# Kernel optimization log

Hardware: AMD Instinct MI355X
Metric: run time of the kernel (lower is better)

Reference implementation:

```python
import jax, jax.numpy as jnp
import numpy as np

HEAD_COUNT = 16
EMBED_DIM = 2048
B, S = 2, 2048


def setup_inputs() -> dict:
    key = jax.random.key(0)
    k1, k2, k3, k4, k5 = jax.random.split(key, 5)
    keys = jax.random.normal(k1, (B, S, EMBED_DIM), dtype=jnp.float32)
    values = jax.random.normal(k2, (B, S, EMBED_DIM), dtype=jnp.float32)
    queries = jax.random.normal(k3, (B, S, EMBED_DIM), dtype=jnp.float32)
    # padding-style mask; guarantee at least one valid key per batch row
    attention_mask = jax.random.randint(k4, (B, S), 0, 2).astype(bool)
    attention_mask = attention_mask.at[:, 0].set(True)
    w_out = jax.random.normal(k5, (EMBED_DIM, EMBED_DIM), dtype=jnp.float32) * (EMBED_DIM ** -0.5)
    return {"keys": keys, "values": values, "queries": queries,
            "attention_mask": attention_mask, "w_out": w_out}


def reference(keys, values, queries, attention_mask, w_out):
    b, s, e = queries.shape
    h = HEAD_COUNT
    c = e // h  # head dim
    k = keys.reshape(b, s, h, c)
    v = values.reshape(b, s, h, c)
    q = queries.reshape(b, s, h, c) * (c ** -0.5)
    # [B,H,Q,K] scores + additive padding bias on key axis
    scores = jnp.einsum('bqhc,bkhc->bhqk', q, k)
    bias = jnp.where(attention_mask, 0.0, -jnp.inf)[:, None, None, :]
    weights = jax.nn.softmax(scores + bias, axis=-1)
    out = jnp.einsum('bhqk,bkhc->bqhc', weights, v).reshape(b, s, e)
    # nn.Linear(bias=False): y = x @ W^T
    return out @ w_out.T
```

## Files before the change

kernel.cpp:

```cpp
#include <hip/hip_runtime.h>
#include <hip/hip_bf16.h>
#include <math.h>

#define B_ 2
#define S_ 2048
#define E_ 2048
#define H_ 16
#define C_ 128

typedef __attribute__((ext_vector_type(8))) short s8v;
typedef __attribute__((ext_vector_type(4))) float f32x4;
typedef __attribute__((ext_vector_type(2))) unsigned u32x2;
typedef __attribute__((ext_vector_type(4))) unsigned u32x4;

#define MFMA16(a, b, c) __builtin_amdgcn_mfma_f32_16x16x32_bf16((a), (b), (c), 0, 0, 0)

__device__ __forceinline__ unsigned fbits(float f) {
    union { float f; unsigned u; } v{f};
    return v.u;
}
__device__ __forceinline__ short f2bfh(float f) {
    return (short)((fbits(f) + 0x8000u) >> 16);
}
__device__ __forceinline__ unsigned bfpack(float lo, float hi) {
    return __builtin_amdgcn_perm(fbits(hi) + 0x8000u, fbits(lo) + 0x8000u, 0x07060302u);
}

__device__ __forceinline__ float fexp2(float x) {
    float r;
    asm("v_exp_f32 %0, %1" : "=v"(r) : "v"(x));
    return r;
}
__device__ __forceinline__ float frcp(float x) {
    float r;
    asm("v_rcp_f32 %0, %1" : "=v"(r) : "v"(x));
    return r;
}

__device__ __forceinline__ void glds16(const void* g, void* l) {
    __builtin_amdgcn_global_load_lds(
        (const __attribute__((address_space(1))) void*)g,
        (__attribute__((address_space(3))) void*)l, 16, 0, 0);
}

template <bool DOK>
__global__ __launch_bounds__(256) void prep_kv(
    const float* __restrict__ K, const float* __restrict__ V,
    short* __restrict__ Kb, short* __restrict__ Vt)
{
    __shared__ __align__(16) short vt[C_][66];
    const int t  = threadIdx.x;
    const int s0 = blockIdx.x * 64;
    const int bh = blockIdx.y;
    const int b = bh >> 4, h = bh & 15;

    if (DOK) {
#pragma unroll
        for (int i = 0; i < 8; ++i) {
            int idx = t + i * 256;
            int s = idx >> 5, c4 = idx & 31;
            float4 v = *(const float4*)(K + ((size_t)(b * S_ + s0 + s)) * E_ + h * C_ + c4 * 4);
            u32x2 o = {bfpack(v.x, v.y), bfpack(v.z, v.w)};
            *(u32x2*)(Kb + ((size_t)(bh * S_ + s0 + s)) * C_ + c4 * 4) = o;
        }
    }
#pragma unroll
    for (int i = 0; i < 8; ++i) {
        int idx = t + i * 256;
        int r = idx >> 5, c4 = idx & 31;
        float4 v = *(const float4*)(V + ((size_t)(b * S_ + s0 + r)) * E_ + h * C_ + c4 * 4);
        vt[c4 * 4 + 0][r] = f2bfh(v.x);
        vt[c4 * 4 + 1][r] = f2bfh(v.y);
        vt[c4 * 4 + 2][r] = f2bfh(v.z);
        vt[c4 * 4 + 3][r] = f2bfh(v.w);
    }
    __syncthreads();
#pragma unroll
    for (int i = 0; i < 4; ++i) {
        int idx = t + i * 256;
        int c = idx >> 3, sc = idx & 7;
        *(s8v*)(Vt + ((size_t)(bh * C_ + c)) * S_ + s0 + sc * 8) = *(const s8v*)&vt[c][sc * 8];
    }
}

__global__ __launch_bounds__(256) void convw_kernel(
    const float* __restrict__ W, short* __restrict__ Wb)
{
    size_t i = ((size_t)blockIdx.x * 256 + threadIdx.x) * 8;
    float4 a = *(const float4*)(W + i);
    float4 b = *(const float4*)(W + i + 4);
    u32x4 o = {bfpack(a.x, a.y), bfpack(a.z, a.w), bfpack(b.x, b.y), bfpack(b.z, b.w)};
    *(u32x4*)(Wb + i) = o;
}

constexpr int QT = 256;
constexpr int KT = 64;
constexpr float M0 = 16.0f;

template <bool KBF16>
__global__ __launch_bounds__(512, 2) void attn_mfma(
    const short* __restrict__ Kb, const float* __restrict__ Kf,
    const float* __restrict__ Qp, const short* __restrict__ Vt,
    const int* __restrict__ maskp, short* __restrict__ Op)
{
    __shared__ __align__(16) short ks[2][KT * 128];
    __shared__ __align__(16) short vs[2][C_ * 64];
    __shared__ __align__(16) short ps[8][16][72];

    const int t = threadIdx.x;
    const int w = t >> 6, lane = t & 63;
    const int c15 = lane & 15, quad = lane >> 4;
    const int q0 = blockIdx.x * QT;
    const int h = blockIdx.y, b = blockIdx.z;
    const int bh = b * H_ + h;

    const float qscale = 0.12751744458187936f;
    s8v qf[2][4];
#pragma unroll
    for (int mi = 0; mi < 2; ++mi) {
        const float* qrow = Qp + ((size_t)(b * S_ + q0 + w * 32 + mi * 16 + c15)) * E_ + h * C_;
#pragma unroll
        for (int kk = 0; kk < 4; ++kk) {
            const float* p = qrow + kk * 32 + quad * 8;
            float4 x0 = *(const float4*)p;
            float4 x1 = *(const float4*)(p + 4);
            u32x4 pk = {bfpack(x0.x * qscale, x0.y * qscale),
                        bfpack(x0.z * qscale, x0.w * qscale),
                        bfpack(x1.x * qscale, x1.y * qscale),
                        bfpack(x1.z * qscale, x1.w * qscale)};
            qf[mi][kk] = *(s8v*)&pk;
        }
    }

    s8v ones;
#pragma unroll
    for (int j = 0; j < 8; ++j) ones[j] = (short)0x3F80;

    f32x4 O[2][8], Ol[2];
#pragma unroll
    for (int mi = 0; mi < 2; ++mi) {
        Ol[mi] = (f32x4){0.f, 0.f, 0.f, 0.f};
#pragma unroll
        for (int ct = 0; ct < 8; ++ct) O[mi][ct] = (f32x4){0.f, 0.f, 0.f, 0.f};
    }

    const short* Kbh = Kb + (size_t)(bh * S_) * C_;
    const float* Kfh = Kf + (size_t)(b * S_) * E_ + h * C_;
    const short* Vbh = Vt + (size_t)(bh * C_) * S_;
    const int*   mptr = maskp + b * S_ + 4 * c15;

    int kgp[4], vgp[2];
#pragma unroll
    for (int kk = 0; kk < 4; ++kk) kgp[kk] = ((4 * kk + quad) ^ c15) * 8;
#pragma unroll
    for (int ks2 = 0; ks2 < 2; ++ks2) vgp[ks2] = ((4 * ks2 + quad) ^ (c15 & 7)) * 8;

    auto stage = [&](short* ksb, short* vsb, int k0) {
        const int r4 = lane >> 4, gp = lane & 15;
#pragma unroll
        for (int i = 0; i < 2; ++i) {
            int row = w * 8 + i * 4 + r4;
            int g = gp ^ ((row >> 2) & 15);
            glds16(Kbh + (size_t)(k0 + row) * C_ + g * 8, ksb + (w * 8 + i * 4) * 128);
        }
        const int cr = lane >> 3, gp7 = lane & 7;
#pragma unroll
        for (int i = 0; i < 2; ++i) {
            int c = w * 16 + i * 8 + cr;
            int g = gp7 ^ (c & 7);
            glds16(Vbh + (size_t)c * S_ + k0 + g * 8, vsb + (w * 16 + i * 8) * 64);
        }
    };

    auto compute = [&](const short* ksc, const short* vsc, int4 mv) {
        float bva[4] = {mv.x ? -M0 : -1e30f, mv.y ? -M0 : -1e30f,
                        mv.z ? -M0 : -1e30f, mv.w ? -M0 : -1e30f};
        f32x4 Sf[2][4];
        __builtin_amdgcn_s_setprio(1);
#pragma unroll
        for (int nt = 0; nt < 4; ++nt) {
            f32x4 s0 = (f32x4){bva[nt], bva[nt], bva[nt], bva[nt]};
            f32x4 s1 = s0;
            const short* krow = ksc + (4 * c15 + nt) * 128;
#pragma unroll
            for (int kk = 0; kk < 4; ++kk) {
                s8v bf = *(const s8v*)(krow + kgp[kk]);
                s0 = MFMA16(qf[0][kk], bf, s0);
                s1 = MFMA16(qf[1][kk], bf, s1);
            }
            Sf[0][nt] = s0; Sf[1][nt] = s1;
        }
        __builtin_amdgcn_s_setprio(0);

        s8v af[2][2];
#pragma unroll
        for (int mi = 0; mi < 2; ++mi) {
#pragma unroll
            for (int r = 0; r < 4; ++r) {
                float p0 = fexp2(Sf[mi][0][r]);
                float p1 = fexp2(Sf[mi][1][r]);
                float p2 = fexp2(Sf[mi][2][r]);
                float p3 = fexp2(Sf[mi][3][r]);
                u32x2 d = {bfpack(p0, p1), bfpack(p2, p3)};
                *(u32x2*)&ps[w][quad * 4 + r][4 * c15] = d;
            }
#pragma unroll
            for (int ks2 = 0; ks2 < 2; ++ks2)
                af[mi][ks2] = *(const s8v*)&ps[w][c15][ks2 * 32 + quad * 8];
        }

        __builtin_amdgcn_s_setprio(1);
#pragma unroll
        for (int ct = 0; ct < 8; ++ct) {
            const short* vrow = vsc + (ct * 16 + c15) * 64;
#pragma unroll
            for (int ks2 = 0; ks2 < 2; ++ks2) {
                s8v bf = *(const s8v*)(vrow + vgp[ks2]);
                O[0][ct] = MFMA16(af[0][ks2], bf, O[0][ct]);
                O[1][ct] = MFMA16(af[1][ks2], bf, O[1][ct]);
            }
        }
#pragma unroll
        for (int mi = 0; mi < 2; ++mi) {
            Ol[mi] = MFMA16(af[mi][0], ones, Ol[mi]);
            Ol[mi] = MFMA16(af[mi][1], ones, Ol[mi]);
        }
        __builtin_amdgcn_s_setprio(0);
    };

    if (KBF16) {
        stage(&ks[0][0], &vs[0][0], 0);
        int4 mcur = *(const int4*)mptr;
        __syncthreads();
#pragma unroll 1
        for (int k0 = 0; k0 < S_; k0 += 2 * KT) {
            stage(&ks[1][0], &vs[1][0], k0 + KT);
            int4 m1 = *(const int4*)(mptr + k0 + KT);
            compute(&ks[0][0], &vs[0][0], mcur);
            __syncthreads();

            int4 m2 = m1;
            if (k0 + 2 * KT < S_) {
                stage(&ks[0][0], &vs[0][0], k0 + 2 * KT);
                m2 = *(const int4*)(mptr + k0 + 2 * KT);
            }
            compute(&ks[1][0], &vs[1][0], m1);
            mcur = m2;
            __syncthreads();
        }
    } else {
#pragma unroll 1
        for (int k0 = 0; k0 < S_; k0 += KT) {
#pragma unroll
            for (int i = 0; i < 4; ++i) {
                int idx = t + i * 512;
                int r = idx >> 5, c4 = idx & 31;
                float4 kv = *(const float4*)(Kfh + (size_t)(k0 + r) * E_ + c4 * 4);
                u32x2 sv = {bfpack(kv.x, kv.y), bfpack(kv.z, kv.w)};
                int gpw = (c4 >> 1) ^ ((r >> 2) & 15);
                *(u32x2*)&ks[0][r * 128 + gpw * 8 + (c4 & 1) * 4] = sv;
            }
            {
                const int cr = lane >> 3, gp7 = lane & 7;
#pragma unroll
                for (int i = 0; i < 2; ++i) {
                    int c = w * 16 + i * 8 + cr;
                    int g = gp7 ^ (c & 7);
                    glds16(Vbh + (size_t)c * S_ + k0 + g * 8, &vs[0][(w * 16 + i * 8) * 64]);
                }
            }
            int4 mv = *(const int4*)(mptr + k0);
            __syncthreads();
            compute(&ks[0][0], &vs[0][0], mv);
            __syncthreads();
        }
    }

#pragma unroll
    for (int mi = 0; mi < 2; ++mi) {
        float inv[4];
#pragma unroll
        for (int r = 0; r < 4; ++r) inv[r] = frcp(Ol[mi][r]);
        size_t rbase = (size_t)(b * S_ + q0 + w * 32 + mi * 16 + quad * 4) * E_ + h * C_;
#pragma unroll
        for (int ct = 0; ct < 8; ++ct)
#pragma unroll
            for (int r = 0; r < 4; ++r)
                Op[rbase + (size_t)r * E_ + ct * 16 + c15] = f2bfh(O[mi][ct][r] * inv[r]);
    }
}

template <bool WBF16>
__global__ __launch_bounds__(512, 2) void proj_mfma(
    const short* __restrict__ X, const short* __restrict__ Wb,
    const float* __restrict__ Wf, float* __restrict__ Y)
{
    __shared__ __align__(16) short As[2][128 * 64];
    __shared__ __align__(16) short Bs[2][256 * 64];

    const int t = threadIdx.x;
    const int w = t >> 6, lane = t & 63;
    const int c15 = lane & 15, quad = lane >> 4;
    const int bm = blockIdx.x * 128, bn = blockIdx.y * 256;
    const int wm = (w >> 2) * 64, wn = (w & 3) * 64;

    f32x4 acc[4][4];
#pragma unroll
    for (int mi = 0; mi < 4; ++mi)
#pragma unroll
        for (int ni = 0; ni < 4; ++ni) acc[mi][ni] = (f32x4){0.f, 0.f, 0.f, 0.f};

    int agp[2];
#pragma unroll
    for (int kk = 0; kk < 2; ++kk) agp[kk] = ((4 * kk + quad) ^ (c15 & 7)) * 8;

    auto stageAB = [&](short* Ab, short* Bb, int k0) {
        const int r8 = lane >> 3, gp = lane & 7;
#pragma unroll
        for (int i = 0; i < 2; ++i) {
            int row = w * 16 + i * 8 + r8;
            int g = gp ^ (row & 7);
            glds16(X + (size_t)(bm + row) * E_ + k0 + g * 8, Ab + (w * 16 + i * 8) * 64);
        }
#pragma unroll
        for (int i = 0; i < 4; ++i) {
            int row = w * 32 + i * 8 + r8;
            int g = gp ^ (row & 7);
            glds16(Wb + (size_t)(bn + row) * E_ + k0 + g * 8, Bb + (w * 32 + i * 8) * 64);
        }
    };

    auto compute = [&](const short* Ab, const short* Bb) {
#pragma unroll
        for (int kk = 0; kk < 2; ++kk) {
            s8v a[4], bb[4];
#pragma unroll
            for (int mi = 0; mi < 4; ++mi)
                a[mi] = *(const s8v*)(Ab + (wm + mi * 16 + c15) * 64 + agp[kk]);
#pragma unroll
            for (int ni = 0; ni < 4; ++ni)
                bb[ni] = *(const s8v*)(Bb + (wn + ni * 16 + c15) * 64 + agp[kk]);
#pragma unroll
            for (int mi = 0; mi < 4; ++mi)
#pragma unroll
                for (int ni = 0; ni < 4; ++ni)
                    acc[mi][ni] = MFMA16(a[mi], bb[ni], acc[mi][ni]);
        }
    };

    if (WBF16) {
        stageAB(&As[0][0], &Bs[0][0], 0);
        __syncthreads();
#pragma unroll 1
        for (int k0 = 0; k0 < E_; k0 += 128) {
            stageAB(&As[1][0], &Bs[1][0], k0 + 64);
            compute(&As[0][0], &Bs[0][0]);
            __syncthreads();

            if (k0 + 128 < E_) stageAB(&As[0][0], &Bs[0][0], k0 + 128);
            compute(&As[1][0], &Bs[1][0]);
            __syncthreads();
        }
    } else {
#pragma unroll 1
        for (int k0 = 0; k0 < E_; k0 += 64) {
            {
                const int r8 = lane >> 3, gp = lane & 7;
#pragma unroll
                for (int i = 0; i < 2; ++i) {
                    int row = w * 16 + i * 8 + r8;
                    int g = gp ^ (row & 7);
                    glds16(X + (size_t)(bm + row) * E_ + k0 + g * 8, &As[0][(w * 16 + i * 8) * 64]);
                }
            }
#pragma unroll
            for (int i = 0; i < 8; ++i) {
                int idx = t + i * 512;
                int r = idx >> 4, c4 = idx & 15;
                float4 wv = *(const float4*)(Wf + (size_t)(bn + r) * E_ + k0 + c4 * 4);
                u32x2 sv = {bfpack(wv.x, wv.y), bfpack(wv.z, wv.w)};
                int gpw = (c4 >> 1) ^ (r & 7);
                *(u32x2*)&Bs[0][r * 64 + gpw * 8 + (c4 & 1) * 4] = sv;
            }
            __syncthreads();
            compute(&As[0][0], &Bs[0][0]);
            __syncthreads();
        }
    }

#pragma unroll
    for (int mi = 0; mi < 4; ++mi)
#pragma unroll
        for (int ni = 0; ni < 4; ++ni) {
            size_t rbase = (size_t)(bm + wm + mi * 16 + quad * 4) * E_ + bn + wn + ni * 16 + c15;
#pragma unroll
            for (int r = 0; r < 4; ++r) Y[rbase + (size_t)r * E_] = acc[mi][ni][r];
        }
}

extern "C" void kernel_launch(void* const* d_in, const int* in_sizes, int n_in,
                              void* d_out, int out_size, void* d_ws, size_t ws_size,
                              hipStream_t stream) {
    const float* keys    = (const float*)d_in[0];
    const float* values  = (const float*)d_in[1];
    const float* queries = (const float*)d_in[2];
    const int*   mask    = (const int*)d_in[3];
    const float* w_out   = (const float*)d_in[4];
    float* out = (float*)d_out;

    const size_t EL = (size_t)B_ * S_ * E_;
    short* ws  = (short*)d_ws;
    short* VtW = ws;
    short* Xb  = ws + EL;
    short* Kb  = ws + 2 * EL;
    short* Wb  = ws + 3 * EL;

    const bool hasK = ws_size >= (3 * EL) * 2;
    const bool hasW = ws_size >= (3 * EL + (size_t)E_ * E_) * 2;

    if (hasK)
        prep_kv<true><<<dim3(S_ / 64, B_ * H_), 256, 0, stream>>>(keys, values, Kb, VtW);
    else
        prep_kv<false><<<dim3(S_ / 64, B_ * H_), 256, 0, stream>>>(keys, values, Kb, VtW);
    if (hasW) convw_kernel<<<(E_ * E_ / 8) / 256, 256, 0, stream>>>(w_out, Wb);

    if (hasK)
        attn_mfma<true><<<dim3(S_ / QT, H_, B_), 512, 0, stream>>>(Kb, keys, queries, VtW, mask, Xb);
    else
        attn_mfma<false><<<dim3(S_ / QT, H_, B_), 512, 0, stream>>>(Kb, keys, queries, VtW, mask, Xb);

    if (hasW)
        proj_mfma<true><<<dim3((B_ * S_) / 128, E_ / 256), 512, 0, stream>>>(Xb, Wb, w_out, out);
    else
        proj_mfma<false><<<dim3((B_ * S_) / 128, E_ / 256), 512, 0, stream>>>(Xb, Wb, w_out, out);
}
```

Before: 269.4 us.

## Use triple-buffered LDS pipeline with partial vmcnt waits in attention and projection

```diff
diff --git a/kernel.cpp b/kernel.cpp
--- a/kernel.cpp
+++ b/kernel.cpp
@@ -103,8 +103,8 @@
     const float* __restrict__ Qp, const short* __restrict__ Vt,
     const int* __restrict__ maskp, short* __restrict__ Op)
 {
-    __shared__ __align__(16) short ks[2][KT * 128];
-    __shared__ __align__(16) short vs[2][C_ * 64];
+    __shared__ __align__(16) short ks[3][KT * 128];
+    __shared__ __align__(16) short vs[3][C_ * 64];
     __shared__ __align__(16) short ps[8][16][72];
 
     const int t = threadIdx.x;
@@ -229,24 +229,29 @@
     };
 
     if (KBF16) {
+        constexpr int NT = S_ / KT;
         stage(&ks[0][0], &vs[0][0], 0);
-        int4 mcur = *(const int4*)mptr;
-        __syncthreads();
+        int4 mv = *(const int4*)mptr;
+        stage(&ks[1][0], &vs[1][0], KT);
+        asm volatile("s_waitcnt vmcnt(5)" ::: "memory");
+        __builtin_amdgcn_s_barrier();
 #pragma unroll 1
-        for (int k0 = 0; k0 < S_; k0 += 2 * KT) {
-            stage(&ks[1][0], &vs[1][0], k0 + KT);
-            int4 m1 = *(const int4*)(mptr + k0 + KT);
-            compute(&ks[0][0], &vs[0][0], mcur);
-            __syncthreads();
-
-            int4 m2 = m1;
-            if (k0 + 2 * KT < S_) {
-                stage(&ks[0][0], &vs[0][0], k0 + 2 * KT);
-                m2 = *(const int4*)(mptr + k0 + 2 * KT);
-            }
-            compute(&ks[1][0], &vs[1][0], m1);
-            mcur = m2;
-            __syncthreads();
+        for (int i = 0; i < NT; ++i) {
+            const int bi = i % 3;
+            int4 mnv = mv;
+            if (i + 2 < NT) {
+                const int bs = (i + 2) % 3;
+                stage(&ks[bs][0], &vs[bs][0], (i + 2) * KT);
+                mnv = *(const int4*)(mptr + (i + 1) * KT);
+                compute(&ks[bi][0], &vs[bi][0], mv);
+                asm volatile("s_waitcnt vmcnt(5)" ::: "memory");
+            } else {
+                if (i + 1 < NT) mnv = *(const int4*)(mptr + (i + 1) * KT);
+                compute(&ks[bi][0], &vs[bi][0], mv);
+                asm volatile("s_waitcnt vmcnt(0)" ::: "memory");
+            }
+            __builtin_amdgcn_s_barrier();
+            mv = mnv;
         }
     } else {
 #pragma unroll 1
@@ -295,8 +300,8 @@
     const short* __restrict__ X, const short* __restrict__ Wb,
     const float* __restrict__ Wf, float* __restrict__ Y)
 {
-    __shared__ __align__(16) short As[2][128 * 64];
-    __shared__ __align__(16) short Bs[2][256 * 64];
+    __shared__ __align__(16) short As[3][128 * 64];
+    __shared__ __align__(16) short Bs[3][256 * 64];
 
     const int t = threadIdx.x;
     const int w = t >> 6, lane = t & 63;
@@ -349,17 +354,24 @@
     };
 
     if (WBF16) {
+        constexpr int NT = E_ / 64;
         stageAB(&As[0][0], &Bs[0][0], 0);
-        __syncthreads();
+        stageAB(&As[1][0], &Bs[1][0], 64);
+        asm volatile("s_waitcnt vmcnt(6)" ::: "memory");
+        __builtin_amdgcn_s_barrier();
 #pragma unroll 1
-        for (int k0 = 0; k0 < E_; k0 += 128) {
-            stageAB(&As[1][0], &Bs[1][0], k0 + 64);
-            compute(&As[0][0], &Bs[0][0]);
-            __syncthreads();
-
-            if (k0 + 128 < E_) stageAB(&As[0][0], &Bs[0][0], k0 + 128);
-            compute(&As[1][0], &Bs[1][0]);
-            __syncthreads();
+        for (int i = 0; i < NT; ++i) {
+            const int bi = i % 3;
+            if (i + 2 < NT) {
+                const int bs = (i + 2) % 3;
+                stageAB(&As[bs][0], &Bs[bs][0], (i + 2) * 64);
+                compute(&As[bi][0], &Bs[bi][0]);
+                asm volatile("s_waitcnt vmcnt(6)" ::: "memory");
+            } else {
+                compute(&As[bi][0], &Bs[bi][0]);
+                asm volatile("s_waitcnt vmcnt(0)" ::: "memory");
+            }
+            __builtin_amdgcn_s_barrier();
         }
     } else {
 #pragma unroll 1
```

After: 283.5 us. 5.2% more time.
